# Performance work log

Hardware: AMD Instinct MI355X
Metric: run time of the kernel (lower is better)

## Reference

```python
import jax, jax.numpy as jnp
import numpy as np

N_IN = 50000
N_OUT = 50000
DEG = 16
E = N_OUT * DEG
C = 64
F = 64


def cartesian_to_spherical(cart, extents):
    # cart: [E,3]
    r_plane_2 = cart[..., 0] ** 2 + cart[..., 1] ** 2
    r_2 = r_plane_2 + cart[..., 2] ** 2
    r_safe = jnp.maximum(jnp.sqrt(r_2), 1e-10)
    cos_phi = cart[..., 2] / r_safe
    r_plane_safe = jnp.maximum(jnp.sqrt(r_plane_2), 1e-10)
    sin_theta = cart[..., 1] / r_plane_safe
    cos_theta = cart[..., 0] / r_plane_safe
    r_normalized = r_safe / extents
    return jnp.stack([r_normalized, cos_phi, sin_theta, cos_theta], axis=-1)  # [E,4]


def setup_inputs() -> dict:
    key = jax.random.key(0)
    k1, k2, k3, k4, k5 = jax.random.split(key, 5)
    input_features = jax.random.normal(k1, (N_IN, C), dtype=jnp.float32)
    input_positions = jax.random.uniform(k2, (N_IN, 3), dtype=jnp.float32)
    output_positions = jax.random.uniform(k3, (N_OUT, 3), dtype=jnp.float32)
    extents = jnp.ones((1,), dtype=jnp.float32)
    kernel = jax.random.normal(k4, (4, C, F), dtype=jnp.float32) * (1.0 / np.sqrt(C))
    bias = jnp.zeros((F,), dtype=jnp.float32)
    neighbors_index = jax.random.randint(k5, (E,), 0, N_IN, dtype=jnp.int32)
    neighbors_row_splits = (DEG * jnp.arange(N_OUT + 1)).astype(jnp.int32)
    return {
        "input_features": input_features,
        "input_positions": input_positions,
        "output_positions": output_positions,
        "extents": extents,
        "kernel": kernel,
        "bias": bias,
        "neighbors_index": neighbors_index,
        "neighbors_row_splits": neighbors_row_splits,
    }


def reference(input_features, input_positions, output_positions, extents,
              kernel, bias, neighbors_index, neighbors_row_splits):
    n_out = output_positions.shape[0]
    n_edges = neighbors_index.shape[0]
    counts = neighbors_row_splits[1:] - neighbors_row_splits[:-1]  # [N_out]
    # segment id of each edge (which output point it belongs to)
    seg_ids = jnp.repeat(jnp.arange(n_out), counts, total_repeat_length=n_edges)
    expanded_query = output_positions[seg_ids]                     # [E,3]
    difference = input_positions[neighbors_index] - expanded_query  # [E,3]
    sph = cartesian_to_spherical(difference, extents)              # [E,4]
    neighbors_feats = input_features[neighbors_index]              # [E,C]
    # contract features with kernel over C first -> [E,4,F] (avoids [E,C,F])
    tmp = jnp.einsum('ec,scf->esf', neighbors_feats, kernel)
    out_edge = jnp.einsum('es,esf->ef', sph, tmp)                  # [E,F]
    out_features = jax.ops.segment_sum(out_edge, seg_ids, num_segments=n_out)
    out_features = out_features + bias
    return out_features
```

## Files before the change

### kernel.cpp

```cpp
#include <hip/hip_runtime.h>

typedef unsigned short u16;
typedef unsigned int u32;
typedef __attribute__((ext_vector_type(2))) _Float16 h2;
typedef __attribute__((ext_vector_type(8))) _Float16 h8;
typedef __attribute__((ext_vector_type(4))) float f32x4;

#define BLOCK 128

__device__ __forceinline__ u16 f2h(float f) {
    union { _Float16 h; u16 u; } v; v.h = (_Float16)f; return v.u;
}

__global__ __launch_bounds__(256)
void prep_all(const float* __restrict__ feats, const float* __restrict__ kmat,
              u16* __restrict__ fh, u16* __restrict__ kbg, int n8) {
    const int id = blockIdx.x * 256 + threadIdx.x;
    if (id < n8) {
        const float4 a = ((const float4*)feats)[2 * id];
        const float4 b = ((const float4*)feats)[2 * id + 1];
        union { u16 h[8]; int4 v; } p;
        p.h[0] = f2h(a.x); p.h[1] = f2h(a.y); p.h[2] = f2h(a.z); p.h[3] = f2h(a.w);
        p.h[4] = f2h(b.x); p.h[5] = f2h(b.y); p.h[6] = f2h(b.z); p.h[7] = f2h(b.w);
        ((int4*)fh)[id] = p.v;
    }
    if (id < 16384) {
        const int k = id >> 6, n = id & 63;
        const int kstep = k >> 5, quad = (k >> 3) & 3, j = k & 7;
        const int ntile = n >> 4, lanep = (quad << 4) | (n & 15);
        kbg[((((ntile << 3) | kstep) << 6) | lanep) * 8 + j] = f2h(kmat[id]);
    }
}

template<bool WS>
__global__ __launch_bounds__(BLOCK, 8)
void sphconv_tile(const float* __restrict__ featsf,
                  const u16* __restrict__ fh,
                  const u16* __restrict__ kbg,
                  const float* __restrict__ in_pos,
                  const float* __restrict__ out_pos,
                  const float* __restrict__ extents,
                  const float* __restrict__ kmat,
                  const float* __restrict__ bias,
                  const int* __restrict__ nidx,
                  const int* __restrict__ rsplits,
                  float* __restrict__ out,
                  int n_out, int n_edges)
{
    __shared__ __align__(16) _Float16 sphT[16][17][8];
    __shared__ int      idxT[16][17];
    __shared__ __align__(16) float redT[4][64][4];

    const int tid = threadIdx.x;
    const int kh  = tid >> 6;
    const int lane = tid & 63;
    const int m = lane & 15, quad = lane >> 4;
    const int obase = blockIdx.x << 4;

    const float inv_ext = __fdividef(1.f, extents[0]);

    #pragma unroll
    for (int u = 0; u < 2; ++u) {
        const int slot = (u << 7) | tid;
        const int mm = slot >> 4, t = slot & 15;
        const int o  = obase + mm;
        const int oc = min(o, n_out - 1);
        const int e0 = rsplits[oc], e1 = rsplits[oc + 1];
        const int e  = e0 + t;
        const bool v = (o < n_out) && (e < e1);
        const int id = nidx[min(e, n_edges - 1)];
        const float dx = in_pos[id * 3 + 0] - out_pos[oc * 3 + 0];
        const float dy = in_pos[id * 3 + 1] - out_pos[oc * 3 + 1];
        const float dz = in_pos[id * 3 + 2] - out_pos[oc * 3 + 2];
        const float rp2 = dx * dx + dy * dy;
        const float r2  = rp2 + dz * dz;
        const float ir  = __builtin_amdgcn_rsqf(fmaxf(r2,  1e-20f));
        const float irp = __builtin_amdgcn_rsqf(fmaxf(rp2, 1e-20f));
        const float rs  = r2 * ir;
        const _Float16 w0 = (_Float16)(v ? rs * inv_ext : 0.f);
        const _Float16 w1 = (_Float16)(v ? dz * ir      : 0.f);
        const _Float16 w2 = (_Float16)(v ? dy * irp     : 0.f);
        const _Float16 w3 = (_Float16)(v ? dx * irp     : 0.f);
        union { _Float16 hh[8]; uint4 v4; } pk;
        pk.hh[0] = w0; pk.hh[1] = w0;
        pk.hh[2] = w1; pk.hh[3] = w1;
        pk.hh[4] = w2; pk.hh[5] = w2;
        pk.hh[6] = w3; pk.hh[7] = w3;
        idxT[t][mm] = id;
        *(uint4*)&sphT[t][mm][0] = pk.v4;
    }
    __syncthreads();

    h2 acc2[4][4];
    #pragma unroll
    for (int s = 0; s < 4; ++s)
        #pragma unroll
        for (int p = 0; p < 4; ++p) acc2[s][p] = (h2)(_Float16)0.f;

    const u16* __restrict__ fbase = fh + (kh << 5) + (quad << 3);
    const float* __restrict__ ffbase = featsf + (kh << 5) + (quad << 3);

    #pragma unroll 2
    for (int t = 0; t < 16; ++t) {
        const int idx = idxT[t][m];
        union { uint4 v4; h2 h[4]; } sp;
        sp.v4 = *(const uint4*)&sphT[t][m][0];
        union { uint4 v4; h2 h[4]; } fw;
        if constexpr (WS) {
            fw.v4 = *(const uint4*)(fbase + (idx << 6));
        } else {
            const float* fr = ffbase + (idx << 6);
            const float4 a0 = *(const float4*)fr;
            const float4 a1 = *(const float4*)(fr + 4);
            fw.h[0] = (h2){(_Float16)a0.x, (_Float16)a0.y};
            fw.h[1] = (h2){(_Float16)a0.z, (_Float16)a0.w};
            fw.h[2] = (h2){(_Float16)a1.x, (_Float16)a1.y};
            fw.h[3] = (h2){(_Float16)a1.z, (_Float16)a1.w};
        }
        #pragma unroll
        for (int s = 0; s < 4; ++s) {
            const h2 ws = sp.h[s];
            #pragma unroll
            for (int p = 0; p < 4; ++p)
                acc2[s][p] = fw.h[p] * ws + acc2[s][p];
        }
    }

    h8 afr[4];
    #pragma unroll
    for (int s = 0; s < 4; ++s) {
        union { h2 h[4]; h8 v; } u;
        #pragma unroll
        for (int p = 0; p < 4; ++p) u.h[p] = acc2[s][p];
        afr[s] = u.v;
    }

    f32x4 C[4] = {{0,0,0,0},{0,0,0,0},{0,0,0,0},{0,0,0,0}};
    #pragma unroll
    for (int nt = 0; nt < 4; ++nt) {
        h8 b[4];
        #pragma unroll
        for (int s = 0; s < 4; ++s) {
            const int ks = (s << 1) | kh;
            if constexpr (WS) {
                b[s] = *(const h8*)(kbg + ((((nt << 3) | ks) << 6) | lane) * 8);
            } else {
                union { u16 hh[8]; h8 v; } p;
                #pragma unroll
                for (int j = 0; j < 8; ++j) {
                    const int k = (ks << 5) | (quad << 3) | j;
                    const int n = (nt << 4) | m;
                    p.hh[j] = f2h(kmat[k * 64 + n]);
                }
                b[s] = p.v;
            }
        }
        #pragma unroll
        for (int s = 0; s < 4; ++s)
            C[nt] = __builtin_amdgcn_mfma_f32_16x16x32_f16(afr[s], b[s], C[nt], 0, 0, 0);
    }

    if (kh == 1) {
        #pragma unroll
        for (int nt = 0; nt < 4; ++nt)
            *(f32x4*)&redT[nt][lane][0] = C[nt];
    }
    __syncthreads();
    if (kh == 0) {
        #pragma unroll
        for (int nt = 0; nt < 4; ++nt) {
            const f32x4 P = *(const f32x4*)&redT[nt][lane][0];
            const int f = (nt << 4) | m;
            const float bv = bias[f];
            #pragma unroll
            for (int r = 0; r < 4; ++r) {
                const int oo = obase + (quad << 2) + r;
                if (oo < n_out) out[(oo << 6) | f] = C[nt][r] + P[r] + bv;
            }
        }
    }
}

extern "C" void kernel_launch(void* const* d_in, const int* in_sizes, int n_in,
                              void* d_out, int out_size, void* d_ws, size_t ws_size,
                              hipStream_t stream) {
    const float* feats   = (const float*)d_in[0];
    const float* in_pos  = (const float*)d_in[1];
    const float* out_pos = (const float*)d_in[2];
    const float* extents = (const float*)d_in[3];
    const float* kmat    = (const float*)d_in[4];
    const float* bias    = (const float*)d_in[5];
    const int*   nidx    = (const int*)d_in[6];
    const int*   rsplits = (const int*)d_in[7];
    const int n_out   = in_sizes[7] - 1;
    const int n_edges = in_sizes[6];
    const int ntiles  = (n_out + 15) >> 4;

    const size_t fh_bytes = (size_t)in_sizes[0] * 2;
    const size_t need = fh_bytes + 32768;
    if (ws_size >= need && (in_sizes[0] & 7) == 0) {
        u16* fh  = (u16*)d_ws;
        u16* kbg = (u16*)((char*)d_ws + fh_bytes);
        const int n8 = in_sizes[0] / 8;
        const int pmax = n8 > 16384 ? n8 : 16384;
        prep_all<<<(pmax + 255) / 256, 256, 0, stream>>>(feats, kmat, fh, kbg, n8);
        sphconv_tile<true><<<ntiles, BLOCK, 0, stream>>>(
            feats, fh, kbg, in_pos, out_pos, extents, kmat, bias, nidx, rsplits,
            (float*)d_out, n_out, n_edges);
    } else {
        sphconv_tile<false><<<ntiles, BLOCK, 0, stream>>>(
            feats, nullptr, nullptr, in_pos, out_pos, extents, kmat, bias, nidx, rsplits,
            (float*)d_out, n_out, n_edges);
    }
}
```

Before: 104.9 us.

## Pad positions to float4 in prep and process two tiles per 256-thread block

```diff
diff --git a/kernel.cpp b/kernel.cpp
--- a/kernel.cpp
+++ b/kernel.cpp
@@ -6,7 +6,7 @@
 typedef __attribute__((ext_vector_type(8))) _Float16 h8;
 typedef __attribute__((ext_vector_type(4))) float f32x4;
 
-#define BLOCK 128
+#define BLOCK 256
 
 __device__ __forceinline__ u16 f2h(float f) {
     union { _Float16 h; u16 u; } v; v.h = (_Float16)f; return v.u;
@@ -14,7 +14,10 @@
 
 __global__ __launch_bounds__(256)
 void prep_all(const float* __restrict__ feats, const float* __restrict__ kmat,
-              u16* __restrict__ fh, u16* __restrict__ kbg, int n8) {
+              const float* __restrict__ in_pos, const float* __restrict__ out_pos,
+              u16* __restrict__ fh, u16* __restrict__ kbg,
+              float4* __restrict__ inp4, float4* __restrict__ outp4,
+              int n8, int n_inp, int n_outp) {
     const int id = blockIdx.x * 256 + threadIdx.x;
     if (id < n8) {
         const float4 a = ((const float4*)feats)[2 * id];
@@ -30,6 +33,10 @@
         const int ntile = n >> 4, lanep = (quad << 4) | (n & 15);
         kbg[((((ntile << 3) | kstep) << 6) | lanep) * 8 + j] = f2h(kmat[id]);
     }
+    if (id < n_inp)
+        inp4[id] = make_float4(in_pos[3 * id], in_pos[3 * id + 1], in_pos[3 * id + 2], 0.f);
+    if (id < n_outp)
+        outp4[id] = make_float4(out_pos[3 * id], out_pos[3 * id + 1], out_pos[3 * id + 2], 0.f);
 }
 
 template<bool WS>
@@ -37,6 +44,8 @@
 void sphconv_tile(const float* __restrict__ featsf,
                   const u16* __restrict__ fh,
                   const u16* __restrict__ kbg,
+                  const float4* __restrict__ inp4,
+                  const float4* __restrict__ outp4,
                   const float* __restrict__ in_pos,
                   const float* __restrict__ out_pos,
                   const float* __restrict__ extents,
@@ -47,31 +56,40 @@
                   float* __restrict__ out,
                   int n_out, int n_edges)
 {
-    __shared__ __align__(16) _Float16 sphT[16][17][8];
-    __shared__ int      idxT[16][17];
-    __shared__ __align__(16) float redT[4][64][4];
+    __shared__ __align__(16) _Float16 sphT[2][16][17][8];
+    __shared__ int      idxT[2][16][17];
+    __shared__ __align__(16) float redT[2][4][64][4];
 
     const int tid = threadIdx.x;
-    const int kh  = tid >> 6;
+    const int th  = tid >> 7;
+    const int kh  = (tid >> 6) & 1;
     const int lane = tid & 63;
     const int m = lane & 15, quad = lane >> 4;
-    const int obase = blockIdx.x << 4;
+    const int obase = (((blockIdx.x << 1) | th) << 4);
 
     const float inv_ext = __fdividef(1.f, extents[0]);
 
     #pragma unroll
     for (int u = 0; u < 2; ++u) {
-        const int slot = (u << 7) | tid;
-        const int mm = slot >> 4, t = slot & 15;
-        const int o  = obase + mm;
+        const int slot = (u << 8) | tid;
+        const int tt = slot >> 8;
+        const int mm = (slot >> 4) & 15, t = slot & 15;
+        const int o  = (((blockIdx.x << 1) | tt) << 4) + mm;
         const int oc = min(o, n_out - 1);
         const int e0 = rsplits[oc], e1 = rsplits[oc + 1];
         const int e  = e0 + t;
         const bool v = (o < n_out) && (e < e1);
         const int id = nidx[min(e, n_edges - 1)];
-        const float dx = in_pos[id * 3 + 0] - out_pos[oc * 3 + 0];
-        const float dy = in_pos[id * 3 + 1] - out_pos[oc * 3 + 1];
-        const float dz = in_pos[id * 3 + 2] - out_pos[oc * 3 + 2];
+        float dx, dy, dz;
+        if constexpr (WS) {
+            const float4 ip = inp4[id];
+            const float4 op = outp4[oc];
+            dx = ip.x - op.x; dy = ip.y - op.y; dz = ip.z - op.z;
+        } else {
+            dx = in_pos[id * 3 + 0] - out_pos[oc * 3 + 0];
+            dy = in_pos[id * 3 + 1] - out_pos[oc * 3 + 1];
+            dz = in_pos[id * 3 + 2] - out_pos[oc * 3 + 2];
+        }
         const float rp2 = dx * dx + dy * dy;
         const float r2  = rp2 + dz * dz;
         const float ir  = __builtin_amdgcn_rsqf(fmaxf(r2,  1e-20f));
@@ -86,8 +104,8 @@
         pk.hh[2] = w1; pk.hh[3] = w1;
         pk.hh[4] = w2; pk.hh[5] = w2;
         pk.hh[6] = w3; pk.hh[7] = w3;
-        idxT[t][mm] = id;
-        *(uint4*)&sphT[t][mm][0] = pk.v4;
+        idxT[tt][t][mm] = id;
+        *(uint4*)&sphT[tt][t][mm][0] = pk.v4;
     }
     __syncthreads();
 
@@ -102,9 +120,9 @@
 
     #pragma unroll 2
     for (int t = 0; t < 16; ++t) {
-        const int idx = idxT[t][m];
+        const int idx = idxT[th][t][m];
         union { uint4 v4; h2 h[4]; } sp;
-        sp.v4 = *(const uint4*)&sphT[t][m][0];
+        sp.v4 = *(const uint4*)&sphT[th][t][m][0];
         union { uint4 v4; h2 h[4]; } fw;
         if constexpr (WS) {
             fw.v4 = *(const uint4*)(fbase + (idx << 6));
@@ -163,13 +181,13 @@
     if (kh == 1) {
         #pragma unroll
         for (int nt = 0; nt < 4; ++nt)
-            *(f32x4*)&redT[nt][lane][0] = C[nt];
+            *(f32x4*)&redT[th][nt][lane][0] = C[nt];
     }
     __syncthreads();
     if (kh == 0) {
         #pragma unroll
         for (int nt = 0; nt < 4; ++nt) {
-            const f32x4 P = *(const f32x4*)&redT[nt][lane][0];
+            const f32x4 P = *(const f32x4*)&redT[th][nt][lane][0];
             const int f = (nt << 4) | m;
             const float bv = bias[f];
             #pragma unroll
@@ -195,21 +213,35 @@
     const int n_out   = in_sizes[7] - 1;
     const int n_edges = in_sizes[6];
     const int ntiles  = (n_out + 15) >> 4;
-
-    const size_t fh_bytes = (size_t)in_sizes[0] * 2;
-    const size_t need = fh_bytes + 32768;
+    const int nblk    = (ntiles + 1) >> 1;
+
+    const int n_inp  = in_sizes[1] / 3;
+    const int n_outp = in_sizes[2] / 3;
+
+    const size_t fh_bytes  = (size_t)in_sizes[0] * 2;
+    const size_t kbg_bytes = 32768;
+    const size_t ip4_bytes = (size_t)n_inp * 16;
+    const size_t op4_bytes = (size_t)n_outp * 16;
+    const size_t need = fh_bytes + kbg_bytes + ip4_bytes + op4_bytes;
+
     if (ws_size >= need && (in_sizes[0] & 7) == 0) {
-        u16* fh  = (u16*)d_ws;
-        u16* kbg = (u16*)((char*)d_ws + fh_bytes);
+        char* w = (char*)d_ws;
+        u16*    fh    = (u16*)w;                    w += fh_bytes;
+        u16*    kbg   = (u16*)w;                    w += kbg_bytes;
+        float4* inp4  = (float4*)w;                 w += ip4_bytes;
+        float4* outp4 = (float4*)w;
         const int n8 = in_sizes[0] / 8;
-        const int pmax = n8 > 16384 ? n8 : 16384;
-        prep_all<<<(pmax + 255) / 256, 256, 0, stream>>>(feats, kmat, fh, kbg, n8);
-        sphconv_tile<true><<<ntiles, BLOCK, 0, stream>>>(
-            feats, fh, kbg, in_pos, out_pos, extents, kmat, bias, nidx, rsplits,
-            (float*)d_out, n_out, n_edges);
+        int pmax = n8 > 16384 ? n8 : 16384;
+        if (n_inp  > pmax) pmax = n_inp;
+        if (n_outp > pmax) pmax = n_outp;
+        prep_all<<<(pmax + 255) / 256, 256, 0, stream>>>(
+            feats, kmat, in_pos, out_pos, fh, kbg, inp4, outp4, n8, n_inp, n_outp);
+        sphconv_tile<true><<<nblk, BLOCK, 0, stream>>>(
+            feats, fh, kbg, inp4, outp4, in_pos, out_pos, extents, kmat, bias,
+            nidx, rsplits, (float*)d_out, n_out, n_edges);
     } else {
-        sphconv_tile<false><<<ntiles, BLOCK, 0, stream>>>(
-            feats, nullptr, nullptr, in_pos, out_pos, extents, kmat, bias, nidx, rsplits,
-            (float*)d_out, n_out, n_edges);
-    }
-}
+        sphconv_tile<false><<<nblk, BLOCK, 0, stream>>>(
+            feats, nullptr, nullptr, nullptr, nullptr, in_pos, out_pos, extents, kmat, bias,
+            nidx, rsplits, (float*)d_out, n_out, n_edges);
+    }
+}
```

Result: slower. 107.1 us (+2.1%).
